# Kernel tuning notes

Measured on AMD Instinct MI355X. Metric: run time of the kernel, lower is better.

Reference implementation:

```python
import jax, jax.numpy as jnp
import numpy as np

NUM_CLASSES = 512


def setup_inputs() -> dict:
    key = jax.random.key(0)
    k1, k2 = jax.random.split(key)
    support_data = jax.random.normal(k1, (2560, 64, 5, 5), dtype=jnp.float32)
    query_data = jax.random.normal(k2, (8192, 64, 5, 5), dtype=jnp.float32)
    # every class 0..511 appears exactly 5 times (sorted, like unique() ordering)
    support_label = (jnp.arange(2560, dtype=jnp.int32) // 5).astype(jnp.int32)
    return {"support_data": support_data, "query_data": query_data,
            "support_label": support_label}


def reference(support_data, query_data, support_label):
    # embedding_net == identity: embeddings are the raw (N, C, H, W) tensors.
    n_q = query_data.shape[0]
    d = support_data.shape[1] * support_data.shape[2] * support_data.shape[3]
    s = support_data.reshape(support_data.shape[0], d)   # [Ns, d]
    q = query_data.reshape(n_q, d)                        # [Nq, d]

    # class-mean prototypes (scatter-mean == per-unique-label mean loop)
    sums = jax.ops.segment_sum(s, support_label, num_segments=NUM_CLASSES)      # [M, d]
    counts = jax.ops.segment_sum(jnp.ones((s.shape[0],), s.dtype),
                                 support_label, num_segments=NUM_CLASSES)       # [M]
    protos = sums / counts[:, None]                                             # [M, d]

    # squared euclidean distance: ||q||^2 + ||p||^2 - 2 q.p  (same math as
    # broadcast (q - p)**2 summed over c,h,w, without the [Nq,M,d] intermediate)
    q2 = jnp.sum(q * q, axis=1, keepdims=True)            # [Nq, 1]
    p2 = jnp.sum(protos * protos, axis=1)                 # [M]
    dist = q2 + p2[None, :] - 2.0 * (q @ protos.T)        # [Nq, M]

    return jax.nn.log_softmax(-dist, axis=1)
```

## Files before the change

kernel.cpp:

```cpp
#include <hip/hip_runtime.h>
#include <hip/hip_bf16.h>
#include <cstdint>
#include <cstddef>

#define NS 2560
#define NQ 8192
#define NC 512
#define DD 1600

typedef __bf16 bf16_t;
typedef __bf16 bf16x4 __attribute__((ext_vector_type(4)));
typedef __bf16 bf16x8 __attribute__((ext_vector_type(8)));
typedef float f32x4 __attribute__((ext_vector_type(4)));

__global__ __launch_bounds__(256) void proto_kernel(
    const float* __restrict__ sup, const int* __restrict__ lab,
    bf16_t* __restrict__ protos, float* __restrict__ p2)
{
    const int m   = blockIdx.x;
    const int tid = threadIdx.x;
    __shared__ int   idxs[32];
    __shared__ int   cnt;
    __shared__ float wsum[4];
    if (tid == 0) cnt = 0;
    __syncthreads();
    for (int i = tid; i < NS; i += 256) {
        if (lab[i] == m) {
            int p = atomicAdd(&cnt, 1);
            if (p < 32) idxs[p] = i;
        }
    }
    __syncthreads();
    int n = cnt < 32 ? cnt : 32;
    if (tid == 0 && n > 1) {
        for (int a = 1; a < n; ++a) {
            int key = idxs[a]; int b = a - 1;
            while (b >= 0 && idxs[b] > key) { idxs[b+1] = idxs[b]; --b; }
            idxs[b+1] = key;
        }
    }
    __syncthreads();

    float acc[7];
    #pragma unroll
    for (int u = 0; u < 7; ++u) acc[u] = 0.f;
    for (int t = 0; t < n; ++t) {
        const float* src = sup + (size_t)idxs[t] * DD;
        #pragma unroll
        for (int u = 0; u < 7; ++u) {
            int j = tid + u * 256;
            if (j < DD) acc[u] += src[j];
        }
    }
    float inv = (n > 0) ? 1.f / (float)n : 0.f;
    float psq = 0.f;
    #pragma unroll
    for (int u = 0; u < 7; ++u) {
        int j = tid + u * 256;
        if (j < DD) {
            float p = acc[u] * inv;
            bf16_t pb = (bf16_t)p;
            protos[(size_t)m * DD + j] = pb;
            float pf = (float)pb;
            psq += pf * pf;
        }
    }
    #pragma unroll
    for (int o = 32; o > 0; o >>= 1) psq += __shfl_xor(psq, o);
    int lane = tid & 63, wid = tid >> 6;
    if (lane == 0) wsum[wid] = psq;
    __syncthreads();
    if (tid == 0) p2[m] = wsum[0] + wsum[1] + wsum[2] + wsum[3];
}

__global__ __launch_bounds__(512, 4) void fused_kernel(
    const float* __restrict__ q, const bf16_t* __restrict__ protos,
    const float* __restrict__ p2, float* __restrict__ out)
{
    __shared__ bf16_t As[32 * 64];
    __shared__ bf16_t Bs[512 * 64];

    const int tid  = threadIdx.x;
    const int lane = tid & 63;
    const int wid  = tid >> 6;
    const int r    = lane & 15;
    const int g    = lane >> 4;
    const int m0   = blockIdx.x * 32;

    float p2c[4];
    #pragma unroll
    for (int ni = 0; ni < 4; ++ni) p2c[ni] = p2[wid * 64 + ni * 16 + r];

    f32x4 acc[2][4];
    #pragma unroll
    for (int mi = 0; mi < 2; ++mi)
        #pragma unroll
        for (int ni = 0; ni < 4; ++ni)
            acc[mi][ni] = (f32x4){0.f, 0.f, 0.f, 0.f};

    const int arow = tid >> 4;
    const int acg  = tid & 15;

    for (int it = 0; it < 25; ++it) {
        const int k0 = it * 64;
        {
            float4 f = *(const float4*)(q + (size_t)(m0 + arow) * DD + k0 + acg * 4);
            bf16x4 w;
            w[0] = (bf16_t)f.x; w[1] = (bf16_t)f.y; w[2] = (bf16_t)f.z; w[3] = (bf16_t)f.w;
            int ab = (arow * 128 + acg * 8) ^ ((arow & 7) << 4);
            *(bf16x4*)((char*)As + ab) = w;
        }
        #pragma unroll
        for (int p = 0; p < 8; ++p) {
            int idx = p * 512 + tid;
            int row = idx >> 3;
            int gs  = (idx & 7) ^ (row & 7);
            const bf16_t* src = protos + (size_t)row * DD + k0 + gs * 8;
            char* dst = (char*)Bs + (size_t)(p * 512 + wid * 64) * 16;
            __builtin_amdgcn_global_load_lds(
                (const __attribute__((address_space(1))) void*)src,
                (__attribute__((address_space(3))) void*)dst, 16, 0, 0);
        }
        __syncthreads();
        #pragma unroll
        for (int kk = 0; kk < 2; ++kk) {
            bf16x8 af[2], bfr[4];
            #pragma unroll
            for (int mi = 0; mi < 2; ++mi) {
                int ab = ((mi * 16 + r) * 128 + kk * 64 + g * 16) ^ ((r & 7) << 4);
                af[mi] = *(const bf16x8*)((const char*)As + ab);
            }
            #pragma unroll
            for (int ni = 0; ni < 4; ++ni) {
                int c  = wid * 64 + ni * 16 + r;
                int bb = (c * 128 + kk * 64 + g * 16) ^ ((r & 7) << 4);
                bfr[ni] = *(const bf16x8*)((const char*)Bs + bb);
            }
            #pragma unroll
            for (int mi = 0; mi < 2; ++mi)
                #pragma unroll
                for (int ni = 0; ni < 4; ++ni)
                    acc[mi][ni] = __builtin_amdgcn_mfma_f32_16x16x32_bf16(
                        af[mi], bfr[ni], acc[mi][ni], 0, 0, 0);
        }
        __syncthreads();
    }

    #pragma unroll
    for (int mi = 0; mi < 2; ++mi)
        #pragma unroll
        for (int ni = 0; ni < 4; ++ni)
            #pragma unroll
            for (int j = 0; j < 4; ++j)
                acc[mi][ni][j] = 2.f * acc[mi][ni][j] - p2c[ni];

    float* red  = (float*)As;
    float* gmax = red + 256;
    float* lse  = gmax + 32;

    float rmax[2][4];
    #pragma unroll
    for (int mi = 0; mi < 2; ++mi)
        #pragma unroll
        for (int j = 0; j < 4; ++j) {
            float m = acc[mi][0][j];
            #pragma unroll
            for (int ni = 1; ni < 4; ++ni) m = fmaxf(m, acc[mi][ni][j]);
            rmax[mi][j] = m;
        }
    #pragma unroll
    for (int o = 1; o < 16; o <<= 1)
        #pragma unroll
        for (int mi = 0; mi < 2; ++mi)
            #pragma unroll
            for (int j = 0; j < 4; ++j)
                rmax[mi][j] = fmaxf(rmax[mi][j], __shfl_xor(rmax[mi][j], o));
    if (r == 0) {
        #pragma unroll
        for (int mi = 0; mi < 2; ++mi)
            #pragma unroll
            for (int j = 0; j < 4; ++j)
                red[(mi * 16 + g * 4 + j) * 8 + wid] = rmax[mi][j];
    }
    __syncthreads();
    if (tid < 32) {
        float m = red[tid * 8];
        #pragma unroll
        for (int w = 1; w < 8; ++w) m = fmaxf(m, red[tid * 8 + w]);
        gmax[tid] = m;
    }
    __syncthreads();

    float rsum[2][4];
    #pragma unroll
    for (int mi = 0; mi < 2; ++mi)
        #pragma unroll
        for (int j = 0; j < 4; ++j) {
            float gm = gmax[mi * 16 + g * 4 + j];
            float s = 0.f;
            #pragma unroll
            for (int ni = 0; ni < 4; ++ni) s += expf(acc[mi][ni][j] - gm);
            rsum[mi][j] = s;
        }
    #pragma unroll
    for (int o = 1; o < 16; o <<= 1)
        #pragma unroll
        for (int mi = 0; mi < 2; ++mi)
            #pragma unroll
            for (int j = 0; j < 4; ++j)
                rsum[mi][j] += __shfl_xor(rsum[mi][j], o);
    if (r == 0) {
        #pragma unroll
        for (int mi = 0; mi < 2; ++mi)
            #pragma unroll
            for (int j = 0; j < 4; ++j)
                red[(mi * 16 + g * 4 + j) * 8 + wid] = rsum[mi][j];
    }
    __syncthreads();
    if (tid < 32) {
        float s = 0.f;
        #pragma unroll
        for (int w = 0; w < 8; ++w) s += red[tid * 8 + w];
        lse[tid] = gmax[tid] + logf(s);
    }
    __syncthreads();

    #pragma unroll
    for (int mi = 0; mi < 2; ++mi) {
        #pragma unroll
        for (int j = 0; j < 4; ++j) {
            float l = lse[mi * 16 + g * 4 + j];
            size_t rowoff = (size_t)(m0 + mi * 16 + g * 4 + j) * NC;
            #pragma unroll
            for (int ni = 0; ni < 4; ++ni)
                out[rowoff + wid * 64 + ni * 16 + r] = acc[mi][ni][j] - l;
        }
    }
}

extern "C" void kernel_launch(void* const* d_in, const int* in_sizes, int n_in,
                              void* d_out, int out_size, void* d_ws, size_t ws_size,
                              hipStream_t stream)
{
    const float* sup = (const float*)d_in[0];
    const float* qry = (const float*)d_in[1];
    const int*   lab = (const int*)d_in[2];
    float* out = (float*)d_out;

    char* ws = (char*)d_ws;
    bf16_t* protos = (bf16_t*)ws;
    float*  p2     = (float*)(ws + 1638400);

    proto_kernel<<<NC, 256, 0, stream>>>(sup, lab, protos, p2);
    fused_kernel<<<NQ / 32, 512, 0, stream>>>(qry, protos, p2, out);
}
```

Measured before the change: 60.81 us.

## Double-buffer A and B LDS tiles to overlap global loads with MFMA

Moves the fused GEMM+softmax kernel to ping-pong LDS buffers in dynamic shared memory. Each iteration prefetches the next K-slice of prototypes (global_load_lds) and query rows into the alternate buffer while MFMAs run on the current one. This leaves one barrier per iteration instead of two and hides global-load latency. The cost is roughly 136KB of LDS per block and a lower launch-bounds occupancy hint. With only 256 blocks there is about one block per CU anyway, so the lost occupancy should matter little.

```diff
diff --git a/kernel.cpp b/kernel.cpp
--- a/kernel.cpp
+++ b/kernel.cpp
@@ -73,12 +73,31 @@
     if (tid == 0) p2[m] = wsum[0] + wsum[1] + wsum[2] + wsum[3];
 }
 
-__global__ __launch_bounds__(512, 4) void fused_kernel(
+__device__ __forceinline__ void stage_B(const bf16_t* __restrict__ protos,
+                                        bf16_t* bbuf, int k0, int tid, int wid)
+{
+    #pragma unroll
+    for (int p = 0; p < 8; ++p) {
+        int idx = p * 512 + tid;
+        int row = idx >> 3;
+        int gs  = (idx & 7) ^ (row & 7);
+        const bf16_t* src = protos + (size_t)row * DD + k0 + gs * 8;
+        char* dst = (char*)bbuf + (size_t)(p * 512 + wid * 64) * 16;
+        __builtin_amdgcn_global_load_lds(
+            (const __attribute__((address_space(1))) void*)src,
+            (__attribute__((address_space(3))) void*)dst, 16, 0, 0);
+    }
+}
+
+__global__ __launch_bounds__(512, 2) void fused_kernel(
     const float* __restrict__ q, const bf16_t* __restrict__ protos,
     const float* __restrict__ p2, float* __restrict__ out)
 {
-    __shared__ bf16_t As[32 * 64];
-    __shared__ bf16_t Bs[512 * 64];
+    extern __shared__ char smem[];
+    bf16_t* Bs0 = (bf16_t*)(smem);
+    bf16_t* Bs1 = (bf16_t*)(smem + 65536);
+    bf16_t* As0 = (bf16_t*)(smem + 131072);
+    bf16_t* As1 = (bf16_t*)(smem + 135168);
 
     const int tid  = threadIdx.x;
     const int lane = tid & 63;
@@ -100,41 +119,45 @@
 
     const int arow = tid >> 4;
     const int acg  = tid & 15;
-
-    for (int it = 0; it < 25; ++it) {
-        const int k0 = it * 64;
-        {
-            float4 f = *(const float4*)(q + (size_t)(m0 + arow) * DD + k0 + acg * 4);
-            bf16x4 w;
-            w[0] = (bf16_t)f.x; w[1] = (bf16_t)f.y; w[2] = (bf16_t)f.z; w[3] = (bf16_t)f.w;
-            int ab = (arow * 128 + acg * 8) ^ ((arow & 7) << 4);
-            *(bf16x4*)((char*)As + ab) = w;
-        }
-        #pragma unroll
-        for (int p = 0; p < 8; ++p) {
-            int idx = p * 512 + tid;
-            int row = idx >> 3;
-            int gs  = (idx & 7) ^ (row & 7);
-            const bf16_t* src = protos + (size_t)row * DD + k0 + gs * 8;
-            char* dst = (char*)Bs + (size_t)(p * 512 + wid * 64) * 16;
-            __builtin_amdgcn_global_load_lds(
-                (const __attribute__((address_space(1))) void*)src,
-                (__attribute__((address_space(3))) void*)dst, 16, 0, 0);
-        }
+    const float* aptr = q + (size_t)(m0 + arow) * DD + acg * 4;
+    const int    aoff = (arow * 128 + acg * 8) ^ ((arow & 7) << 4);
+
+    {
+        float4 f = *(const float4*)(aptr);
+        stage_B(protos, Bs0, 0, tid, wid);
+        bf16x4 w;
+        w[0] = (bf16_t)f.x; w[1] = (bf16_t)f.y; w[2] = (bf16_t)f.z; w[3] = (bf16_t)f.w;
+        *(bf16x4*)((char*)As0 + aoff) = w;
         __syncthreads();
+    }
+
+    for (int t = 0; t < 25; ++t) {
+        const int cur = t & 1;
+        bf16_t* bs  = cur ? Bs1 : Bs0;
+        bf16_t* as  = cur ? As1 : As0;
+        bf16_t* bsn = cur ? Bs0 : Bs1;
+        bf16_t* asn = cur ? As0 : As1;
+        const bool pre = (t < 24);
+
+        float4 fA;
+        if (pre) {
+            fA = *(const float4*)(aptr + (t + 1) * 64);
+            stage_B(protos, bsn, (t + 1) * 64, tid, wid);
+        }
+
         #pragma unroll
         for (int kk = 0; kk < 2; ++kk) {
             bf16x8 af[2], bfr[4];
             #pragma unroll
             for (int mi = 0; mi < 2; ++mi) {
                 int ab = ((mi * 16 + r) * 128 + kk * 64 + g * 16) ^ ((r & 7) << 4);
-                af[mi] = *(const bf16x8*)((const char*)As + ab);
+                af[mi] = *(const bf16x8*)((const char*)as + ab);
             }
             #pragma unroll
             for (int ni = 0; ni < 4; ++ni) {
                 int c  = wid * 64 + ni * 16 + r;
                 int bb = (c * 128 + kk * 64 + g * 16) ^ ((r & 7) << 4);
-                bfr[ni] = *(const bf16x8*)((const char*)Bs + bb);
+                bfr[ni] = *(const bf16x8*)((const char*)bs + bb);
             }
             #pragma unroll
             for (int mi = 0; mi < 2; ++mi)
@@ -143,6 +166,13 @@
                     acc[mi][ni] = __builtin_amdgcn_mfma_f32_16x16x32_bf16(
                         af[mi], bfr[ni], acc[mi][ni], 0, 0, 0);
         }
+
+        if (pre) {
+            bf16x4 w;
+            w[0] = (bf16_t)fA.x; w[1] = (bf16_t)fA.y;
+            w[2] = (bf16_t)fA.z; w[3] = (bf16_t)fA.w;
+            *(bf16x4*)((char*)asn + aoff) = w;
+        }
         __syncthreads();
     }
 
@@ -154,7 +184,7 @@
             for (int j = 0; j < 4; ++j)
                 acc[mi][ni][j] = 2.f * acc[mi][ni][j] - p2c[ni];
 
-    float* red  = (float*)As;
+    float* red  = (float*)smem;
     float* gmax = red + 256;
     float* lse  = gmax + 32;
 
@@ -251,6 +281,10 @@
     bf16_t* protos = (bf16_t*)ws;
     float*  p2     = (float*)(ws + 1638400);
 
+    const int smem_bytes = 139264;
+    hipFuncSetAttribute(reinterpret_cast<const void*>(fused_kernel),
+                        hipFuncAttributeMaxDynamicSharedMemorySize, smem_bytes);
+
     proto_kernel<<<NC, 256, 0, stream>>>(sup, lab, protos, p2);
-    fused_kernel<<<NQ / 32, 512, 0, stream>>>(qry, protos, p2, out);
-}
+    fused_kernel<<<NQ / 32, 512, smem_bytes, stream>>>(qry, protos, p2, out);
+}
```

Result: faster. 54.76 us (-10.0%).

## Triple-buffer prototype tiles with async LDS loads and register-direct query fragments

Applied to the files above, without the earlier changes.

Replaces the synchronous two-barrier K loop with a 3-stage software pipeline. Prototype tiles of 32 K-columns stream into three 32KB LDS buffers via global_load_lds, and vmcnt waits let two stages stay in flight. Query rows are now loaded straight from global memory into registers as MFMA fragments, converted to bf16 in registers, and no longer staged through LDS. The cost is 96KB of dynamic shared memory, which limits occupancy to about one block per CU. The B layout also changes to a k-group-major arrangement without XOR swizzling, so LDS bank conflicts may appear.

```diff
diff --git a/kernel.cpp b/kernel.cpp
--- a/kernel.cpp
+++ b/kernel.cpp
@@ -9,7 +9,6 @@
 #define DD 1600
 
 typedef __bf16 bf16_t;
-typedef __bf16 bf16x4 __attribute__((ext_vector_type(4)));
 typedef __bf16 bf16x8 __attribute__((ext_vector_type(8)));
 typedef float f32x4 __attribute__((ext_vector_type(4)));
 
@@ -73,12 +72,74 @@
     if (tid == 0) p2[m] = wsum[0] + wsum[1] + wsum[2] + wsum[3];
 }
 
-__global__ __launch_bounds__(512, 4) void fused_kernel(
+struct ASlot { float4 f[4]; };
+
+__device__ __forceinline__ void issueA(ASlot& s, const float* a0,
+                                       const float* a1, int t)
+{
+    const float* p0 = a0 + t * 32;
+    const float* p1 = a1 + t * 32;
+    s.f[0] = *(const float4*)(p0);
+    s.f[1] = *(const float4*)(p0 + 4);
+    s.f[2] = *(const float4*)(p1);
+    s.f[3] = *(const float4*)(p1 + 4);
+}
+
+__device__ __forceinline__ void issueB(const bf16_t* __restrict__ protos,
+                                       char* buf, int k0, int tid, int wid)
+{
+    #pragma unroll
+    for (int p = 0; p < 4; ++p) {
+        int idx = p * 512 + tid;
+        int c   = idx & 511;
+        int gs  = idx >> 9;
+        const bf16_t* src = protos + (size_t)c * DD + k0 + gs * 8;
+        char* dst = buf + (size_t)(p * 512 + wid * 64) * 16;
+        __builtin_amdgcn_global_load_lds(
+            (const __attribute__((address_space(1))) void*)src,
+            (__attribute__((address_space(3))) void*)dst, 16, 0, 0);
+    }
+}
+
+template<int VM>
+__device__ __forceinline__ void kwait()
+{
+    if constexpr (VM == 12)     asm volatile("s_waitcnt vmcnt(12)" ::: "memory");
+    else if constexpr (VM == 8) asm volatile("s_waitcnt vmcnt(8)"  ::: "memory");
+    else                        asm volatile("s_waitcnt vmcnt(0)"  ::: "memory");
+}
+
+__device__ __forceinline__ void computeT(const char* buf, const ASlot& s,
+                                         f32x4 (&acc)[2][4], int rdoff)
+{
+    bf16x8 af[2];
+    #pragma unroll
+    for (int mi = 0; mi < 2; ++mi) {
+        float4 lo = s.f[2 * mi], hi = s.f[2 * mi + 1];
+        bf16x8 w;
+        w[0] = (bf16_t)lo.x; w[1] = (bf16_t)lo.y;
+        w[2] = (bf16_t)lo.z; w[3] = (bf16_t)lo.w;
+        w[4] = (bf16_t)hi.x; w[5] = (bf16_t)hi.y;
+        w[6] = (bf16_t)hi.z; w[7] = (bf16_t)hi.w;
+        af[mi] = w;
+    }
+    bf16x8 bfr[4];
+    #pragma unroll
+    for (int ni = 0; ni < 4; ++ni)
+        bfr[ni] = *(const bf16x8*)(buf + rdoff + ni * 256);
+    #pragma unroll
+    for (int mi = 0; mi < 2; ++mi)
+        #pragma unroll
+        for (int ni = 0; ni < 4; ++ni)
+            acc[mi][ni] = __builtin_amdgcn_mfma_f32_16x16x32_bf16(
+                af[mi], bfr[ni], acc[mi][ni], 0, 0, 0);
+}
+
+__global__ __launch_bounds__(512, 1) void fused_kernel(
     const float* __restrict__ q, const bf16_t* __restrict__ protos,
     const float* __restrict__ p2, float* __restrict__ out)
 {
-    __shared__ bf16_t As[32 * 64];
-    __shared__ bf16_t Bs[512 * 64];
+    extern __shared__ char smem[];
 
     const int tid  = threadIdx.x;
     const int lane = tid & 63;
@@ -87,9 +148,9 @@
     const int g    = lane >> 4;
     const int m0   = blockIdx.x * 32;
 
-    float p2c[4];
-    #pragma unroll
-    for (int ni = 0; ni < 4; ++ni) p2c[ni] = p2[wid * 64 + ni * 16 + r];
+    const float* ab0 = q + (size_t)(m0 + r) * DD + g * 8;
+    const float* ab1 = ab0 + (size_t)16 * DD;
+    const int rdoff  = g * 8192 + (wid * 64 + r) * 16;
 
     f32x4 acc[2][4];
     #pragma unroll
@@ -98,54 +159,37 @@
         for (int ni = 0; ni < 4; ++ni)
             acc[mi][ni] = (f32x4){0.f, 0.f, 0.f, 0.f};
 
-    const int arow = tid >> 4;
-    const int acg  = tid & 15;
-
-    for (int it = 0; it < 25; ++it) {
-        const int k0 = it * 64;
-        {
-            float4 f = *(const float4*)(q + (size_t)(m0 + arow) * DD + k0 + acg * 4);
-            bf16x4 w;
-            w[0] = (bf16_t)f.x; w[1] = (bf16_t)f.y; w[2] = (bf16_t)f.z; w[3] = (bf16_t)f.w;
-            int ab = (arow * 128 + acg * 8) ^ ((arow & 7) << 4);
-            *(bf16x4*)((char*)As + ab) = w;
-        }
-        #pragma unroll
-        for (int p = 0; p < 8; ++p) {
-            int idx = p * 512 + tid;
-            int row = idx >> 3;
-            int gs  = (idx & 7) ^ (row & 7);
-            const bf16_t* src = protos + (size_t)row * DD + k0 + gs * 8;
-            char* dst = (char*)Bs + (size_t)(p * 512 + wid * 64) * 16;
-            __builtin_amdgcn_global_load_lds(
-                (const __attribute__((address_space(1))) void*)src,
-                (__attribute__((address_space(3))) void*)dst, 16, 0, 0);
-        }
-        __syncthreads();
-        #pragma unroll
-        for (int kk = 0; kk < 2; ++kk) {
-            bf16x8 af[2], bfr[4];
-            #pragma unroll
-            for (int mi = 0; mi < 2; ++mi) {
-                int ab = ((mi * 16 + r) * 128 + kk * 64 + g * 16) ^ ((r & 7) << 4);
-                af[mi] = *(const bf16x8*)((const char*)As + ab);
-            }
-            #pragma unroll
-            for (int ni = 0; ni < 4; ++ni) {
-                int c  = wid * 64 + ni * 16 + r;
-                int bb = (c * 128 + kk * 64 + g * 16) ^ ((r & 7) << 4);
-                bfr[ni] = *(const bf16x8*)((const char*)Bs + bb);
-            }
-            #pragma unroll
-            for (int mi = 0; mi < 2; ++mi)
-                #pragma unroll
-                for (int ni = 0; ni < 4; ++ni)
-                    acc[mi][ni] = __builtin_amdgcn_mfma_f32_16x16x32_bf16(
-                        af[mi], bfr[ni], acc[mi][ni], 0, 0, 0);
-        }
-        __syncthreads();
-    }
-
+    ASlot s0, s1, s2;
+
+    issueA(s0, ab0, ab1, 0);
+    issueB(protos, smem,          0, tid, wid);
+    issueA(s1, ab0, ab1, 1);
+    issueB(protos, smem + 32768, 32, tid, wid);
+
+#define GITER(T, SL, SU, BL, BU, VM, DOPRE)                                   \
+    {                                                                         \
+        if (DOPRE) issueA(SL, ab0, ab1, (T) + 2);                             \
+        kwait<VM>();                                                          \
+        asm volatile("s_barrier" ::: "memory");                               \
+        if (DOPRE) issueB(protos, smem + (size_t)(BL) * 32768,                \
+                          ((T) + 2) * 32, tid, wid);                          \
+        computeT(smem + (size_t)(BU) * 32768, SU, acc, rdoff);                \
+    }
+
+    for (int tt = 0; tt < 48; tt += 3) {
+        GITER(tt,     s2, s0, 2, 0, 12, true);
+        GITER(tt + 1, s0, s1, 0, 1, 12, true);
+        GITER(tt + 2, s1, s2, 1, 2, 12, true);
+    }
+    GITER(48, s2, s0, 2, 0, 8, false);
+    GITER(49, s0, s1, 0, 1, 0, false);
+#undef GITER
+
+    __syncthreads();
+
+    float p2c[4];
+    #pragma unroll
+    for (int ni = 0; ni < 4; ++ni) p2c[ni] = p2[wid * 64 + ni * 16 + r];
     #pragma unroll
     for (int mi = 0; mi < 2; ++mi)
         #pragma unroll
@@ -154,7 +198,7 @@
             for (int j = 0; j < 4; ++j)
                 acc[mi][ni][j] = 2.f * acc[mi][ni][j] - p2c[ni];
 
-    float* red  = (float*)As;
+    float* red  = (float*)smem;
     float* gmax = red + 256;
     float* lse  = gmax + 32;
 
@@ -251,6 +295,10 @@
     bf16_t* protos = (bf16_t*)ws;
     float*  p2     = (float*)(ws + 1638400);
 
+    const int smem_bytes = 98304;
+    hipFuncSetAttribute(reinterpret_cast<const void*>(fused_kernel),
+                        hipFuncAttributeMaxDynamicSharedMemorySize, smem_bytes);
+
     proto_kernel<<<NC, 256, 0, stream>>>(sup, lab, protos, p2);
-    fused_kernel<<<NQ / 32, 512, 0, stream>>>(qry, protos, p2, out);
-}
+    fused_kernel<<<NQ / 32, 512, smem_bytes, stream>>>(qry, protos, p2, out);
+}
```

Measured after the change: 130.6 us. +114.7%, slower.
